# Performance work log

Measured on AMD Instinct MI355X. Metric: run time of the kernel, lower is better.

The kernel has to match this reference:

```python
import jax, jax.numpy as jnp
import numpy as np

EPS = 1e-5

def _conv1x1(x, w, b):
    # x: (B,C,H,W), w: (O,C), b: (O,)
    return jnp.einsum('bchw,oc->bohw', x, w) + b[None, :, None, None]

def _maxpool2(x):
    B, C, H, W = x.shape
    return x.reshape(B, C, H // 2, 2, W // 2, 2).max(axis=(3, 5))

def setup_inputs() -> dict:
    key = jax.random.key(0)
    ks = jax.random.split(key, 12)
    B, C, Ci, H, W = 8, 256, 128, 64, 64
    s = lambda k, shape, scale: jax.random.normal(k, shape, jnp.float32) * scale
    return {
        'x': s(ks[0], (B, C, H, W), 1.0),
        'neighborFeat': s(ks[1], (B, C, H, W), 1.0),
        'g_w': s(ks[2], (Ci, C), 0.05), 'g_b': jnp.zeros((Ci,), jnp.float32),
        'theta_w': s(ks[3], (Ci, C), 0.05), 'theta_b': jnp.zeros((Ci,), jnp.float32),
        'phi_w': s(ks[4], (Ci, C), 0.05), 'phi_b': jnp.zeros((Ci,), jnp.float32),
        'w_w': s(ks[5], (C, Ci), 0.05), 'w_b': jnp.zeros((C,), jnp.float32),
        'bn_gamma': s(ks[6], (C,), 0.1) + 1.0,
        'bn_beta': s(ks[7], (C,), 0.1),
        'bn_mean': s(ks[8], (C,), 0.1),
        'bn_var': jax.random.uniform(ks[9], (C,), jnp.float32, 0.5, 1.5),
    }

def reference(x, neighborFeat, g_w, g_b, theta_w, theta_b, phi_w, phi_b,
              w_w, w_b, bn_gamma, bn_beta, bn_mean, bn_var):
    B, C, H, W = x.shape
    Ci = g_w.shape[0]
    # g: conv1x1 on x then maxpool2 -> (B, Nkv, Ci)
    g_x = _maxpool2(_conv1x1(x, g_w, g_b)).reshape(B, Ci, -1).transpose(0, 2, 1)
    # theta: conv1x1 on neighborFeat, full res -> (B, Nq, Ci)
    theta_x = _conv1x1(neighborFeat, theta_w, theta_b).reshape(B, Ci, -1).transpose(0, 2, 1)
    # phi: conv1x1 on neighborFeat then maxpool2 -> (B, Ci, Nkv)
    phi_x = _maxpool2(_conv1x1(neighborFeat, phi_w, phi_b)).reshape(B, Ci, -1)
    f = jnp.einsum('bqc,bck->bqk', theta_x, phi_x)       # (B, Nq, Nkv)
    f_div_C = jax.nn.softmax(f, axis=-1)
    y = jnp.einsum('bqk,bkc->bqc', f_div_C, g_x)          # (B, Nq, Ci)
    y = y.transpose(0, 2, 1).reshape(B, Ci, H, W)
    # W: conv1x1 + BatchNorm (eval mode with running stats)
    wy = _conv1x1(y, w_w, w_b)
    wy = (wy - bn_mean[None, :, None, None]) * (bn_gamma[None, :, None, None]
          * jax.lax.rsqrt(bn_var + EPS)[None, :, None, None]) + bn_beta[None, :, None, None]
    return wy + x
```

## Files before the change

kernel.cpp:

```cpp
#include <hip/hip_runtime.h>

typedef __attribute__((ext_vector_type(8))) short short8;
typedef __attribute__((ext_vector_type(4))) short short4v;
typedef __attribute__((ext_vector_type(4))) float f32x4;
typedef __attribute__((ext_vector_type(16))) float f32x16;
typedef __attribute__((ext_vector_type(4))) unsigned u32x4;

__device__ __forceinline__ float bf2f(short s) {
  union { unsigned u; float f; } cv;
  cv.u = ((unsigned)(unsigned short)s) << 16;
  return cv.f;
}
__device__ __forceinline__ short f2bf(float f) {
  union { float f; unsigned u; } cv;
  cv.f = f;
  unsigned r = (cv.u + 0x7fffu + ((cv.u >> 16) & 1u)) >> 16;
  return (short)(unsigned short)r;
}
__device__ __forceinline__ unsigned pk2(float a, float b) {
  return (unsigned)(unsigned short)f2bf(a) | ((unsigned)(unsigned short)f2bf(b) << 16);
}

#define MFMA16(a, b, c) __builtin_amdgcn_mfma_f32_16x16x32_bf16((a), (b), (c), 0, 0, 0)
#define MFMA32(a, b, c) __builtin_amdgcn_mfma_f32_32x32x16_bf16((a), (b), (c), 0, 0, 0)

__global__ __launch_bounds__(256) void cvt_w(
    const float* __restrict__ s0, const float* __restrict__ s1,
    const float* __restrict__ s2, const float* __restrict__ s3,
    short* __restrict__ d)
{
  const float* srcs[4] = {s0, s1, s2, s3};
  const float* s = srcs[blockIdx.y];
  int i = (blockIdx.x * 256 + threadIdx.x) * 4;
  f32x4 v = *reinterpret_cast<const f32x4*>(s + i);
  short4v o;
  #pragma unroll
  for (int j = 0; j < 4; j++) o[j] = f2bf(v[j]);
  *reinterpret_cast<short4v*>(d + (size_t)blockIdx.y * 32768 + i) = o;
}

template <int NPROJ, int MODE1>
__global__ __launch_bounds__(512) void conv_proj(
    const float* __restrict__ in,
    const short* __restrict__ w0, const float* __restrict__ bias0,
    const short* __restrict__ w1, const float* __restrict__ bias1,
    short* __restrict__ out0, short* __restrict__ out1)
{
  __shared__ short in_t[128][40];
  __shared__ short wt[NPROJ][128][40];

  const int b = blockIdx.y;
  const int p0 = blockIdx.x * 128;
  const int tid = threadIdx.x;
  const int wave = tid >> 6, lane = tid & 63;
  const int lr = lane & 15, lg = lane >> 4;

  const short* wsrc[2] = {w0, w1};

  f32x4 acc[NPROJ][8];
  #pragma unroll
  for (int pj = 0; pj < NPROJ; pj++)
    #pragma unroll
    for (int n = 0; n < 8; n++) acc[pj][n] = (f32x4)0.0f;

  for (int kc = 0; kc < 256; kc += 32) {
    __syncthreads();
    {
      int c = tid >> 4;
      int pg = (tid & 15) * 8;
      const float* src = in + ((size_t)(b * 256 + kc + c)) * 4096 + p0 + pg;
      f32x4 v0 = *reinterpret_cast<const f32x4*>(src);
      f32x4 v1 = *reinterpret_cast<const f32x4*>(src + 4);
      #pragma unroll
      for (int j = 0; j < 8; j++) {
        int p = pg + j;
        int a = ((p & 63) >> 1) * 4 + ((p >> 6) << 1) + (p & 1);
        float fv = (j < 4) ? v0[j] : v1[j - 4];
        in_t[a][c ^ ((((a >> 3) & 3)) << 3)] = f2bf(fv);
      }
    }
    if (tid < NPROJ * 128) {
      int pj = tid >> 7, o = tid & 127;
      const short8* src = reinterpret_cast<const short8*>(wsrc[pj] + (size_t)o * 256 + kc);
      int f = (o >> 3) & 3;
      #pragma unroll
      for (int gq = 0; gq < 4; gq++)
        *reinterpret_cast<short8*>(&wt[pj][o][(gq ^ f) * 8]) = src[gq];
    }
    __syncthreads();

    int arow = wave * 16 + lr;
    short8 afrag = *reinterpret_cast<const short8*>(
        &in_t[arow][(lg ^ ((arow >> 3) & 3)) * 8]);
    #pragma unroll
    for (int pj = 0; pj < NPROJ; pj++) {
      #pragma unroll
      for (int n = 0; n < 8; n++) {
        int brow = n * 16 + lr;
        short8 bfrag = *reinterpret_cast<const short8*>(
            &wt[pj][brow][(lg ^ ((brow >> 3) & 3)) * 8]);
        acc[pj][n] = MFMA16(afrag, bfrag, acc[pj][n]);
      }
    }
  }

  const float* bsrc[2] = {bias0, bias1};
  short* osrc[2] = {out0, out1};
  const int kp = blockIdx.x * 32 + wave * 4 + lg;
  #pragma unroll
  for (int pj = 0; pj < NPROJ; pj++) {
    const int mode = (pj == 0 && NPROJ == 2) ? 0 : MODE1;
    #pragma unroll
    for (int n = 0; n < 8; n++) {
      int o = n * 16 + lr;
      float bv = bsrc[pj][o];
      if (mode == 0) {
        #pragma unroll
        for (int r = 0; r < 4; r++) {
          int pix = (wave * 4 + lg) * 2 + (r & 1) + ((r >> 1) & 1) * 64;
          osrc[pj][((size_t)b * 4096 + p0 + pix) * 128 + o] = f2bf(acc[pj][n][r] + bv);
        }
      } else {
        f32x4 v = acc[pj][n];
        float pv = fmaxf(fmaxf(v[0], v[1]), fmaxf(v[2], v[3])) + bv;
        if (mode == 1)
          osrc[pj][((size_t)b * 1024 + kp) * 128 + o] = f2bf(pv);
        else
          osrc[pj][((size_t)b * 128 + o) * 1024 + kp] = f2bf(pv);
      }
    }
  }
}

__global__ __launch_bounds__(512) void attn_split(
    const short* __restrict__ theta, const short* __restrict__ phi,
    const short* __restrict__ g,
    short* __restrict__ pacc0, short* __restrict__ pacc1,
    float* __restrict__ pm, float* __restrict__ pl)
{
  __shared__ short phi_s[2][64][128];
  __shared__ short g_s[2][128][64];

  const int b = blockIdx.y, z = blockIdx.z;
  const int q0 = blockIdx.x * 256;
  const int tid = threadIdx.x;
  const int wave = tid >> 6, lane = tid & 63;
  const int l31 = lane & 31, hi = lane >> 5;

  short8 ath[8];
  {
    const short* tq = theta + ((size_t)b * 4096 + q0 + wave * 32 + l31) * 128 + hi * 8;
    #pragma unroll
    for (int s = 0; s < 8; s++)
      ath[s] = *reinterpret_cast<const short8*>(tq + s * 16);
  }

  const int pr = tid >> 3, pc2 = (tid & 7) * 2;
  const int gr = tid >> 2, gc2 = (tid & 3) * 2;
  const short* phi_src = phi + ((size_t)b * 1024 + z * 512 + pr) * 128 + pc2 * 8;
  const short* g_src   = g + ((size_t)b * 128 + gr) * 1024 + z * 512 + gc2 * 8;

  short8 sphi[2], sg[2];
  #pragma unroll
  for (int j = 0; j < 2; j++) {
    sphi[j] = *reinterpret_cast<const short8*>(phi_src + j * 8);
    sg[j]   = *reinterpret_cast<const short8*>(g_src + j * 8);
  }

  float mrun = -1e30f, lpart = 0.0f;
  f32x16 acc[4];
  #pragma unroll
  for (int n = 0; n < 4; n++) acc[n] = (f32x16)0.0f;

  {
    char* pb = (char*)&phi_s[0][0][0];
    char* gb = (char*)&g_s[0][0][0];
    #pragma unroll
    for (int j = 0; j < 2; j++) {
      *reinterpret_cast<short8*>(pb + pr * 256 + (((pc2 + j) ^ (pr & 15)) * 16)) = sphi[j];
      *reinterpret_cast<short8*>(gb + gr * 128 + (((gc2 + j) ^ (gr & 7)) * 16)) = sg[j];
    }
  }

  for (int t = 0; t < 8; t++) {
    __syncthreads();
    char* pb = (char*)&phi_s[t & 1][0][0];
    char* gb = (char*)&g_s[t & 1][0][0];

    if (t < 7) {
      const short* ps = phi_src + (t + 1) * 64 * 128;
      const short* gs = g_src + (t + 1) * 64;
      #pragma unroll
      for (int j = 0; j < 2; j++) {
        sphi[j] = *reinterpret_cast<const short8*>(ps + j * 8);
        sg[j]   = *reinterpret_cast<const short8*>(gs + j * 8);
      }
    }

    f32x16 facc0 = (f32x16)0.0f, facc1 = (f32x16)0.0f;
    __builtin_amdgcn_s_setprio(1);
    #pragma unroll
    for (int s = 0; s < 8; s++) {
      int slot = (s << 1) | hi;
      short8 pf0 = *reinterpret_cast<const short8*>(
          pb + l31 * 256 + ((slot ^ (l31 & 15)) * 16));
      short8 pf1 = *reinterpret_cast<const short8*>(
          pb + (32 + l31) * 256 + ((slot ^ (l31 & 15)) * 16));
      facc0 = MFMA32(pf0, ath[s], facc0);
      facc1 = MFMA32(pf1, ath[s], facc1);
    }
    __builtin_amdgcn_s_setprio(0);

    float m = facc0[0];
    #pragma unroll
    for (int r = 1; r < 16; r++) m = fmaxf(m, facc0[r]);
    #pragma unroll
    for (int r = 0; r < 16; r++) m = fmaxf(m, facc1[r]);
    m = fmaxf(m, __shfl_xor(m, 32));
    if (__any(m - mrun > 10.0f)) {
      float mn = fmaxf(mrun, m);
      float sc = __expf(mrun - mn);
      mrun = mn;
      lpart *= sc;
      #pragma unroll
      for (int reg = 0; reg < 16; reg++) {
        int qr = (reg & 3) + 8 * (reg >> 2) + 4 * hi;
        float sr = __shfl(sc, qr);
        #pragma unroll
        for (int n = 0; n < 4; n++) acc[n][reg] *= sr;
      }
    }
    float ls = 0.0f;
    #pragma unroll
    for (int r = 0; r < 16; r++) { facc0[r] = __expf(facc0[r] - mrun); ls += facc0[r]; }
    #pragma unroll
    for (int r = 0; r < 16; r++) { facc1[r] = __expf(facc1[r] - mrun); ls += facc1[r]; }
    lpart += ls;

    __builtin_amdgcn_s_setprio(1);
    #pragma unroll
    for (int s = 0; s < 4; s++) {
      const int base = (s & 1) * 8;
      float p0, p1, p2, p3, p4, p5, p6, p7;
      if (s < 2) {
        p0 = facc0[base + 0]; p1 = facc0[base + 1]; p2 = facc0[base + 2]; p3 = facc0[base + 3];
        p4 = facc0[base + 4]; p5 = facc0[base + 5]; p6 = facc0[base + 6]; p7 = facc0[base + 7];
      } else {
        p0 = facc1[base + 0]; p1 = facc1[base + 1]; p2 = facc1[base + 2]; p3 = facc1[base + 3];
        p4 = facc1[base + 4]; p5 = facc1[base + 5]; p6 = facc1[base + 6]; p7 = facc1[base + 7];
      }
      unsigned P0w0 = pk2(p0, p1), P0w1 = pk2(p2, p3);
      unsigned P1w0 = pk2(p4, p5), P1w1 = pk2(p6, p7);
      unsigned x0 = (unsigned)__shfl_xor((int)P0w0, 32);
      unsigned x1 = (unsigned)__shfl_xor((int)P0w1, 32);
      unsigned y0 = (unsigned)__shfl_xor((int)P1w0, 32);
      unsigned y1 = (unsigned)__shfl_xor((int)P1w1, 32);
      union { u32x4 u; short8 s8; } pf;
      pf.u[0] = hi ? y0 : P0w0;
      pf.u[1] = hi ? y1 : P0w1;
      pf.u[2] = hi ? P1w0 : x0;
      pf.u[3] = hi ? P1w1 : x1;
      int slot = (s << 1) | hi;
      #pragma unroll
      for (int n = 0; n < 4; n++) {
        int rg = n * 32 + l31;
        short8 gf = *reinterpret_cast<const short8*>(
            gb + rg * 128 + ((slot ^ (rg & 7)) * 16));
        acc[n] = MFMA32(pf.s8, gf, acc[n]);
      }
    }
    __builtin_amdgcn_s_setprio(0);

    if (t < 7) {
      char* pb2 = (char*)&phi_s[(t + 1) & 1][0][0];
      char* gb2 = (char*)&g_s[(t + 1) & 1][0][0];
      #pragma unroll
      for (int j = 0; j < 2; j++) {
        *reinterpret_cast<short8*>(pb2 + pr * 256 + (((pc2 + j) ^ (pr & 15)) * 16)) = sphi[j];
        *reinterpret_cast<short8*>(gb2 + gr * 128 + (((gc2 + j) ^ (gr & 7)) * 16)) = sg[j];
      }
    }
  }

  float lsum = lpart + __shfl_xor(lpart, 32);
  if (lane < 32) {
    int q = q0 + wave * 32 + l31;
    pm[z * 32768 + b * 4096 + q] = mrun;
    pl[z * 32768 + b * 4096 + q] = lsum;
  }
  short* pacc = z ? pacc1 : pacc0;
  #pragma unroll
  for (int n = 0; n < 4; n++) {
    #pragma unroll
    for (int reg = 0; reg < 16; reg++) {
      int q = q0 + wave * 32 + (reg & 3) + 8 * (reg >> 2) + 4 * hi;
      pacc[((size_t)b * 4096 + q) * 128 + n * 32 + l31] = f2bf(acc[n][reg]);
    }
  }
}

__global__ __launch_bounds__(512) void wconv_bn(
    const short* __restrict__ a0, const short* __restrict__ a1,
    const float* __restrict__ pm, const float* __restrict__ pl,
    const short* __restrict__ ww, const float* __restrict__ wb,
    const float* __restrict__ gamma, const float* __restrict__ beta,
    const float* __restrict__ mean, const float* __restrict__ var,
    const float* __restrict__ x, float* __restrict__ out)
{
  __shared__ short y_s[128][136];
  __shared__ float sc_s[256];
  __shared__ float sh_s[256];

  const int b = blockIdx.y;
  const int q0 = blockIdx.x * 128;
  const int tid = threadIdx.x;
  const int wave = tid >> 6, lane = tid & 63;
  const int lr = lane & 15, lg = lane >> 4;

  {
    int r = tid >> 2, c0 = (tid & 3) * 32;
    int iq = b * 4096 + q0 + r;
    float m0 = pm[iq], m1 = pm[32768 + iq];
    float l0 = pl[iq], l1 = pl[32768 + iq];
    float M = fmaxf(m0, m1);
    float w0 = __expf(m0 - M), w1 = __expf(m1 - M);
    float inv = 1.0f / (w0 * l0 + w1 * l1);
    w0 *= inv; w1 *= inv;
    size_t base = (size_t)iq * 128 + c0;
    #pragma unroll
    for (int j = 0; j < 4; j++) {
      short8 A0 = *reinterpret_cast<const short8*>(a0 + base + j * 8);
      short8 A1 = *reinterpret_cast<const short8*>(a1 + base + j * 8);
      short8 o;
      #pragma unroll
      for (int e = 0; e < 8; e++)
        o[e] = f2bf(w0 * bf2f(A0[e]) + w1 * bf2f(A1[e]));
      *reinterpret_cast<short8*>(&y_s[r][c0 + j * 8]) = o;
    }
    if (tid < 256) {
      float s = gamma[tid] * rsqrtf(var[tid] + 1e-5f);
      sc_s[tid] = s;
      sh_s[tid] = (wb[tid] - mean[tid]) * s + beta[tid];
    }
  }
  __syncthreads();

  f32x4 acc[2][8];
  #pragma unroll
  for (int m = 0; m < 2; m++)
    #pragma unroll
    for (int n = 0; n < 8; n++) acc[m][n] = (f32x4)0.0f;

  #pragma unroll
  for (int kk = 0; kk < 4; kk++) {
    short8 af[2], bfr[8];
    #pragma unroll
    for (int m = 0; m < 2; m++)
      af[m] = *reinterpret_cast<const short8*>(
          ww + (size_t)(wave * 32 + m * 16 + lr) * 128 + kk * 32 + lg * 8);
    #pragma unroll
    for (int n = 0; n < 8; n++)
      bfr[n] = *reinterpret_cast<const short8*>(&y_s[n * 16 + lr][kk * 32 + lg * 8]);
    #pragma unroll
    for (int m = 0; m < 2; m++)
      #pragma unroll
      for (int n = 0; n < 8; n++)
        acc[m][n] = MFMA16(af[m], bfr[n], acc[m][n]);
  }

  #pragma unroll
  for (int m = 0; m < 2; m++) {
    #pragma unroll
    for (int n = 0; n < 8; n++) {
      #pragma unroll
      for (int r = 0; r < 4; r++) {
        int co = wave * 32 + m * 16 + lg * 4 + r;
        int q = q0 + n * 16 + lr;
        size_t oidx = ((size_t)b * 256 + co) * 4096 + q;
        float v = acc[m][n][r] * sc_s[co] + sh_s[co];
        out[oidx] = v + x[oidx];
      }
    }
  }
}

extern "C" void kernel_launch(void* const* d_in, const int* in_sizes, int n_in,
                              void* d_out, int out_size, void* d_ws, size_t ws_size,
                              hipStream_t stream)
{
  const float* x    = (const float*)d_in[0];
  const float* nb   = (const float*)d_in[1];
  const float* g_w  = (const float*)d_in[2];
  const float* g_b  = (const float*)d_in[3];
  const float* th_w = (const float*)d_in[4];
  const float* th_b = (const float*)d_in[5];
  const float* ph_w = (const float*)d_in[6];
  const float* ph_b = (const float*)d_in[7];
  const float* w_w  = (const float*)d_in[8];
  const float* w_b  = (const float*)d_in[9];
  const float* gam  = (const float*)d_in[10];
  const float* bet  = (const float*)d_in[11];
  const float* mu   = (const float*)d_in[12];
  const float* var  = (const float*)d_in[13];
  float* out = (float*)d_out;

  char* ws = (char*)d_ws;
  short* theta_full = (short*)(ws);
  short* pacc0      = (short*)(ws + (size_t)(8u << 20));
  short* pacc1      = (short*)(ws + (size_t)(16u << 20));
  short* phi_kc     = (short*)(ws + (size_t)(24u << 20));
  short* g_ck       = (short*)(ws + (size_t)(26u << 20));
  short* wts        = (short*)(ws + (size_t)(36u << 20));
  float* pm         = (float*)(ws + (size_t)(37u << 20));
  float* pl         = (float*)(ws + (size_t)(38u << 20));
  short* th_wb = wts;
  short* ph_wb = wts + 32768;
  short* g_wb  = wts + 2 * 32768;
  short* w_wb  = wts + 3 * 32768;

  cvt_w<<<dim3(32, 4), 256, 0, stream>>>(th_w, ph_w, g_w, w_w, wts);
  conv_proj<2, 1><<<dim3(32, 8), 512, 0, stream>>>(nb, th_wb, th_b, ph_wb, ph_b,
                                                   theta_full, phi_kc);
  conv_proj<1, 2><<<dim3(32, 8), 512, 0, stream>>>(x, g_wb, g_b, nullptr, nullptr,
                                                   g_ck, nullptr);
  attn_split<<<dim3(16, 8, 2), 512, 0, stream>>>(theta_full, phi_kc, g_ck,
                                                 pacc0, pacc1, pm, pl);
  wconv_bn<<<dim3(32, 8), 512, 0, stream>>>(pacc0, pacc1, pm, pl,
                                            w_wb, w_b, gam, bet, mu, var, x, out);
}
```

Before: 89.35 us.

## Merge conv launches and combine split-KV attention halves in-block via LDS

```diff
diff --git a/kernel.cpp b/kernel.cpp
--- a/kernel.cpp
+++ b/kernel.cpp
@@ -40,15 +40,13 @@
 }
 
 template <int NPROJ, int MODE1>
-__global__ __launch_bounds__(512) void conv_proj(
+__device__ __forceinline__ void conv_body(
+    short (*in_t)[40], short (*wt)[40],
     const float* __restrict__ in,
     const short* __restrict__ w0, const float* __restrict__ bias0,
     const short* __restrict__ w1, const float* __restrict__ bias1,
     short* __restrict__ out0, short* __restrict__ out1)
 {
-  __shared__ short in_t[128][40];
-  __shared__ short wt[NPROJ][128][40];
-
   const int b = blockIdx.y;
   const int p0 = blockIdx.x * 128;
   const int tid = threadIdx.x;
@@ -85,7 +83,7 @@
       int f = (o >> 3) & 3;
       #pragma unroll
       for (int gq = 0; gq < 4; gq++)
-        *reinterpret_cast<short8*>(&wt[pj][o][(gq ^ f) * 8]) = src[gq];
+        *reinterpret_cast<short8*>(&wt[pj * 128 + o][(gq ^ f) * 8]) = src[gq];
     }
     __syncthreads();
 
@@ -98,7 +96,7 @@
       for (int n = 0; n < 8; n++) {
         int brow = n * 16 + lr;
         short8 bfrag = *reinterpret_cast<const short8*>(
-            &wt[pj][brow][(lg ^ ((brow >> 3) & 3)) * 8]);
+            &wt[pj * 128 + brow][(lg ^ ((brow >> 3) & 3)) * 8]);
         acc[pj][n] = MFMA16(afrag, bfrag, acc[pj][n]);
       }
     }
@@ -132,37 +130,53 @@
   }
 }
 
-__global__ __launch_bounds__(512) void attn_split(
+__global__ __launch_bounds__(512, 4) void conv_all(
+    const float* __restrict__ nb, const float* __restrict__ x,
+    const short* __restrict__ th_w, const float* __restrict__ th_b,
+    const short* __restrict__ ph_w, const float* __restrict__ ph_b,
+    const short* __restrict__ g_w, const float* __restrict__ g_b,
+    short* __restrict__ theta, short* __restrict__ phi_kc,
+    short* __restrict__ g_ck)
+{
+  __shared__ short in_t[128][40];
+  __shared__ short wt[256][40];
+  if (blockIdx.z == 0)
+    conv_body<2, 1>(in_t, wt, nb, th_w, th_b, ph_w, ph_b, theta, phi_kc);
+  else
+    conv_body<1, 2>(in_t, wt, x, g_w, g_b, nullptr, nullptr, g_ck, nullptr);
+}
+
+__global__ __launch_bounds__(512) void attn(
     const short* __restrict__ theta, const short* __restrict__ phi,
-    const short* __restrict__ g,
-    short* __restrict__ pacc0, short* __restrict__ pacc1,
-    float* __restrict__ pm, float* __restrict__ pl)
-{
-  __shared__ short phi_s[2][64][128];
-  __shared__ short g_s[2][128][64];
-
-  const int b = blockIdx.y, z = blockIdx.z;
-  const int q0 = blockIdx.x * 256;
+    const short* __restrict__ g, short* __restrict__ y)
+{
+  __shared__ char lds[131072];
+  __shared__ float ml[8][32][2];
+
+  const int b = blockIdx.y;
+  const int q0 = blockIdx.x * 128;
   const int tid = threadIdx.x;
   const int wave = tid >> 6, lane = tid & 63;
   const int l31 = lane & 31, hi = lane >> 5;
+  const int zw = wave >> 2, wq = wave & 3;
 
   short8 ath[8];
   {
-    const short* tq = theta + ((size_t)b * 4096 + q0 + wave * 32 + l31) * 128 + hi * 8;
+    const short* tq = theta + ((size_t)b * 4096 + q0 + wq * 32 + l31) * 128 + hi * 8;
     #pragma unroll
     for (int s = 0; s < 8; s++)
       ath[s] = *reinterpret_cast<const short8*>(tq + s * 16);
   }
 
-  const int pr = tid >> 3, pc2 = (tid & 7) * 2;
-  const int gr = tid >> 2, gc2 = (tid & 3) * 2;
-  const short* phi_src = phi + ((size_t)b * 1024 + z * 512 + pr) * 128 + pc2 * 8;
-  const short* g_src   = g + ((size_t)b * 128 + gr) * 1024 + z * 512 + gc2 * 8;
-
-  short8 sphi[2], sg[2];
-  #pragma unroll
-  for (int j = 0; j < 2; j++) {
+  const int t8 = tid & 255, zs = tid >> 8;
+  const int pr = t8 >> 2, pcq = t8 & 3;
+  const int gr = t8 >> 1, ghq = t8 & 1;
+  const short* phi_src = phi + ((size_t)b * 1024 + zs * 512 + pr) * 128 + pcq * 32;
+  const short* g_src   = g + ((size_t)b * 128 + gr) * 1024 + zs * 512 + ghq * 32;
+
+  short8 sphi[4], sg[4];
+  #pragma unroll
+  for (int j = 0; j < 4; j++) {
     sphi[j] = *reinterpret_cast<const short8*>(phi_src + j * 8);
     sg[j]   = *reinterpret_cast<const short8*>(g_src + j * 8);
   }
@@ -173,25 +187,25 @@
   for (int n = 0; n < 4; n++) acc[n] = (f32x16)0.0f;
 
   {
-    char* pb = (char*)&phi_s[0][0][0];
-    char* gb = (char*)&g_s[0][0][0];
-    #pragma unroll
-    for (int j = 0; j < 2; j++) {
-      *reinterpret_cast<short8*>(pb + pr * 256 + (((pc2 + j) ^ (pr & 15)) * 16)) = sphi[j];
-      *reinterpret_cast<short8*>(gb + gr * 128 + (((gc2 + j) ^ (gr & 7)) * 16)) = sg[j];
+    char* pb = lds + zs * 16384;
+    char* gb = lds + 65536 + zs * 16384;
+    #pragma unroll
+    for (int j = 0; j < 4; j++) {
+      *reinterpret_cast<short8*>(pb + pr * 256 + (((pcq * 4 + j) ^ (pr & 15)) * 16)) = sphi[j];
+      *reinterpret_cast<short8*>(gb + gr * 128 + (((ghq * 4 + j) ^ (gr & 7)) * 16)) = sg[j];
     }
   }
 
   for (int t = 0; t < 8; t++) {
     __syncthreads();
-    char* pb = (char*)&phi_s[t & 1][0][0];
-    char* gb = (char*)&g_s[t & 1][0][0];
+    char* pb = lds + ((t & 1) * 2 + zw) * 16384;
+    char* gb = lds + 65536 + ((t & 1) * 2 + zw) * 16384;
 
     if (t < 7) {
       const short* ps = phi_src + (t + 1) * 64 * 128;
       const short* gs = g_src + (t + 1) * 64;
       #pragma unroll
-      for (int j = 0; j < 2; j++) {
+      for (int j = 0; j < 4; j++) {
         sphi[j] = *reinterpret_cast<const short8*>(ps + j * 8);
         sg[j]   = *reinterpret_cast<const short8*>(gs + j * 8);
       }
@@ -272,37 +286,57 @@
     __builtin_amdgcn_s_setprio(0);
 
     if (t < 7) {
-      char* pb2 = (char*)&phi_s[(t + 1) & 1][0][0];
-      char* gb2 = (char*)&g_s[(t + 1) & 1][0][0];
-      #pragma unroll
-      for (int j = 0; j < 2; j++) {
-        *reinterpret_cast<short8*>(pb2 + pr * 256 + (((pc2 + j) ^ (pr & 15)) * 16)) = sphi[j];
-        *reinterpret_cast<short8*>(gb2 + gr * 128 + (((gc2 + j) ^ (gr & 7)) * 16)) = sg[j];
+      char* pb2 = lds + (((t + 1) & 1) * 2 + zs) * 16384;
+      char* gb2 = lds + 65536 + (((t + 1) & 1) * 2 + zs) * 16384;
+      #pragma unroll
+      for (int j = 0; j < 4; j++) {
+        *reinterpret_cast<short8*>(pb2 + pr * 256 + (((pcq * 4 + j) ^ (pr & 15)) * 16)) = sphi[j];
+        *reinterpret_cast<short8*>(gb2 + gr * 128 + (((ghq * 4 + j) ^ (gr & 7)) * 16)) = sg[j];
       }
     }
   }
 
   float lsum = lpart + __shfl_xor(lpart, 32);
-  if (lane < 32) {
-    int q = q0 + wave * 32 + l31;
-    pm[z * 32768 + b * 4096 + q] = mrun;
-    pl[z * 32768 + b * 4096 + q] = lsum;
-  }
-  short* pacc = z ? pacc1 : pacc0;
-  #pragma unroll
-  for (int n = 0; n < 4; n++) {
-    #pragma unroll
-    for (int reg = 0; reg < 16; reg++) {
-      int q = q0 + wave * 32 + (reg & 3) + 8 * (reg >> 2) + 4 * hi;
-      pacc[((size_t)b * 4096 + q) * 128 + n * 32 + l31] = f2bf(acc[n][reg]);
-    }
+  if (lane < 32) { ml[wave][l31][0] = mrun; ml[wave][l31][1] = lsum; }
+  __syncthreads();
+  float mo = ml[wave ^ 4][l31][0];
+  float lo = ml[wave ^ 4][l31][1];
+  float M = fmaxf(mrun, mo);
+  float e0 = __expf(mrun - M), e1 = __expf(mo - M);
+  float wown = e0 / (e0 * lsum + e1 * lo);
+  #pragma unroll
+  for (int reg = 0; reg < 16; reg++) {
+    int qr = (reg & 3) + 8 * (reg >> 2) + 4 * hi;
+    float wr = __shfl(wown, qr);
+    #pragma unroll
+    for (int n = 0; n < 4; n++) acc[n][reg] *= wr;
+  }
+  float* mb = (float*)(lds + wq * 16384);
+  if (zw == 1) {
+    #pragma unroll
+    for (int n = 0; n < 4; n++)
+      #pragma unroll
+      for (int reg = 0; reg < 16; reg++) {
+        int qrow = (reg & 3) + 8 * (reg >> 2) + 4 * hi;
+        mb[qrow * 128 + n * 32 + l31] = acc[n][reg];
+      }
+  }
+  __syncthreads();
+  if (zw == 0) {
+    #pragma unroll
+    for (int n = 0; n < 4; n++)
+      #pragma unroll
+      for (int reg = 0; reg < 16; reg++) {
+        int qrow = (reg & 3) + 8 * (reg >> 2) + 4 * hi;
+        float v = acc[n][reg] + mb[qrow * 128 + n * 32 + l31];
+        y[((size_t)b * 4096 + q0 + wq * 32 + qrow) * 128 + n * 32 + l31] = f2bf(v);
+      }
   }
 }
 
 __global__ __launch_bounds__(512) void wconv_bn(
-    const short* __restrict__ a0, const short* __restrict__ a1,
-    const float* __restrict__ pm, const float* __restrict__ pl,
-    const short* __restrict__ ww, const float* __restrict__ wb,
+    const short* __restrict__ yb, const short* __restrict__ ww,
+    const float* __restrict__ wb,
     const float* __restrict__ gamma, const float* __restrict__ beta,
     const float* __restrict__ mean, const float* __restrict__ var,
     const float* __restrict__ x, float* __restrict__ out)
@@ -319,24 +353,11 @@
 
   {
     int r = tid >> 2, c0 = (tid & 3) * 32;
-    int iq = b * 4096 + q0 + r;
-    float m0 = pm[iq], m1 = pm[32768 + iq];
-    float l0 = pl[iq], l1 = pl[32768 + iq];
-    float M = fmaxf(m0, m1);
-    float w0 = __expf(m0 - M), w1 = __expf(m1 - M);
-    float inv = 1.0f / (w0 * l0 + w1 * l1);
-    w0 *= inv; w1 *= inv;
-    size_t base = (size_t)iq * 128 + c0;
-    #pragma unroll
-    for (int j = 0; j < 4; j++) {
-      short8 A0 = *reinterpret_cast<const short8*>(a0 + base + j * 8);
-      short8 A1 = *reinterpret_cast<const short8*>(a1 + base + j * 8);
-      short8 o;
-      #pragma unroll
-      for (int e = 0; e < 8; e++)
-        o[e] = f2bf(w0 * bf2f(A0[e]) + w1 * bf2f(A1[e]));
-      *reinterpret_cast<short8*>(&y_s[r][c0 + j * 8]) = o;
-    }
+    const short8* src = reinterpret_cast<const short8*>(
+        yb + ((size_t)(b * 4096 + q0 + r)) * 128 + c0);
+    short8* dst = reinterpret_cast<short8*>(&y_s[r][c0]);
+    #pragma unroll
+    for (int j = 0; j < 4; j++) dst[j] = src[j];
     if (tid < 256) {
       float s = gamma[tid] * rsqrtf(var[tid] + 1e-5f);
       sc_s[tid] = s;
@@ -406,25 +427,18 @@
 
   char* ws = (char*)d_ws;
   short* theta_full = (short*)(ws);
-  short* pacc0      = (short*)(ws + (size_t)(8u << 20));
-  short* pacc1      = (short*)(ws + (size_t)(16u << 20));
-  short* phi_kc     = (short*)(ws + (size_t)(24u << 20));
-  short* g_ck       = (short*)(ws + (size_t)(26u << 20));
-  short* wts        = (short*)(ws + (size_t)(36u << 20));
-  float* pm         = (float*)(ws + (size_t)(37u << 20));
-  float* pl         = (float*)(ws + (size_t)(38u << 20));
+  short* yb         = (short*)(ws + (size_t)(8u << 20));
+  short* phi_kc     = (short*)(ws + (size_t)(16u << 20));
+  short* g_ck       = (short*)(ws + (size_t)(18u << 20));
+  short* wts        = (short*)(ws + (size_t)(20u << 20));
   short* th_wb = wts;
   short* ph_wb = wts + 32768;
   short* g_wb  = wts + 2 * 32768;
   short* w_wb  = wts + 3 * 32768;
 
   cvt_w<<<dim3(32, 4), 256, 0, stream>>>(th_w, ph_w, g_w, w_w, wts);
-  conv_proj<2, 1><<<dim3(32, 8), 512, 0, stream>>>(nb, th_wb, th_b, ph_wb, ph_b,
-                                                   theta_full, phi_kc);
-  conv_proj<1, 2><<<dim3(32, 8), 512, 0, stream>>>(x, g_wb, g_b, nullptr, nullptr,
-                                                   g_ck, nullptr);
-  attn_split<<<dim3(16, 8, 2), 512, 0, stream>>>(theta_full, phi_kc, g_ck,
-                                                 pacc0, pacc1, pm, pl);
-  wconv_bn<<<dim3(32, 8), 512, 0, stream>>>(pacc0, pacc1, pm, pl,
-                                            w_wb, w_b, gam, bet, mu, var, x, out);
-}
+  conv_all<<<dim3(32, 8, 2), 512, 0, stream>>>(nb, x, th_wb, th_b, ph_wb, ph_b,
+                                               g_wb, g_b, theta_full, phi_kc, g_ck);
+  attn<<<dim3(32, 8), 512, 0, stream>>>(theta_full, phi_kc, g_ck, yb);
+  wconv_bn<<<dim3(32, 8), 512, 0, stream>>>(yb, w_wb, w_b, gam, bet, mu, var, x, out);
+}
```

Result: faster. 82.44 us (-7.7%).
